# Kernel tuning notes

Measured on AMD Instinct MI355X. Metric: run time of the kernel, lower is better.

The kernel has to match this reference:

```python
import jax, jax.numpy as jnp
import numpy as np

N = 50000      # nodes
E = 800000     # edges (before self-loops)
IN = 64        # in_dim
C = 64         # hidden_dim (per-head out channels)
H = 4          # heads
NEG_SLOPE = 0.2


def setup_inputs() -> dict:
    key = jax.random.key(0)
    ks = jax.random.split(key, 9)
    x = jax.random.normal(ks[0], (N, IN), jnp.float32)
    edge_index = jax.random.randint(ks[1], (2, E), 0, N)
    edge_attr = jax.random.uniform(ks[2], (E, 1), jnp.float32)
    s_in = 1.0 / np.sqrt(IN)
    s_c = 1.0 / np.sqrt(C)
    W = jax.random.normal(ks[3], (IN, H * C), jnp.float32) * s_in
    att_src = jax.random.normal(ks[4], (H, C), jnp.float32) * s_c
    att_dst = jax.random.normal(ks[5], (H, C), jnp.float32) * s_c
    lin_edge_w = jax.random.normal(ks[6], (1, H * C), jnp.float32)
    att_edge = jax.random.normal(ks[7], (H, C), jnp.float32) * s_c
    bias = jnp.zeros((C,), jnp.float32)
    return dict(x=x, edge_index=edge_index, edge_attr=edge_attr, W=W,
                att_src=att_src, att_dst=att_dst, lin_edge_w=lin_edge_w,
                att_edge=att_edge, bias=bias)


def reference(x, edge_index, edge_attr, W, att_src, att_dst, lin_edge_w, att_edge, bias):
    n = x.shape[0]
    # add self-loops (PyG default add_self_loops=True, fill_value='mean')
    loop = jnp.arange(n)
    src = jnp.concatenate([edge_index[0], loop])          # [E+N]
    dst = jnp.concatenate([edge_index[1], loop])          # [E+N]
    ea = jnp.concatenate([edge_attr,
                          jnp.full((n, 1), edge_attr.mean(), edge_attr.dtype)], axis=0)
    # node transform: [N, H, C]
    h = (x @ W).reshape(n, H, C)
    a_src = jnp.einsum('nhc,hc->nh', h, att_src)          # [N, H]
    a_dst = jnp.einsum('nhc,hc->nh', h, att_dst)          # [N, H]
    eh = (ea @ lin_edge_w).reshape(-1, H, C)              # [E+N, H, C]
    a_edge = jnp.einsum('ehc,hc->eh', eh, att_edge)       # [E+N, H]
    # per-edge attention logit
    alpha = a_src[src] + a_dst[dst] + a_edge              # [E+N, H]
    alpha = jax.nn.leaky_relu(alpha, NEG_SLOPE)
    # segment softmax over edges grouped by destination node
    amax = jax.ops.segment_max(alpha, dst, num_segments=n)
    alpha = jnp.exp(alpha - amax[dst])
    asum = jax.ops.segment_sum(alpha, dst, num_segments=n)
    alpha = alpha / (asum[dst] + 1e-16)                   # [E+N, H]
    # weighted message + scatter-add aggregation
    msg = h[src] * alpha[..., None]                       # [E+N, H, C]
    out = jax.ops.segment_sum(msg, dst, num_segments=n)   # [N, H, C]
    out = out.mean(axis=1) + bias                         # concat=False -> head mean
    # ReLU + residual
    return jax.nn.relu(out) + x
```

## Files before the change

kernel.cpp:

```cpp
#include <hip/hip_runtime.h>
#include <hip/hip_fp16.h>
#include <math.h>

#define H 4
#define C 64
#define HC 256
#define NEG 0.2f
#define ROWU 64
#define MAXREC 63
#define XPAD 72
#define HPAD 264
#define BKT 128
#define BSH 7
#define TILE 2048
#define SEG 32
#define SEGSH 5

typedef __attribute__((ext_vector_type(8))) _Float16 half8;
typedef __attribute__((ext_vector_type(4))) float f32x4;
typedef float f32x2 __attribute__((vector_size(8)));

__global__ __launch_bounds__(256) void phase1_kernel(
    const float* __restrict__ x, const float* __restrict__ W,
    const float* __restrict__ att_src, const float* __restrict__ att_dst,
    const int* __restrict__ ei, const float* __restrict__ edge_attr,
    unsigned char* __restrict__ h, float* __restrict__ a_src, float* __restrict__ a_dst,
    uint2* __restrict__ arena, unsigned* __restrict__ counts,
    float* __restrict__ mean_acc, int Nn, int Ee, int G1, int ntile) {
    int t = threadIdx.x;
    if ((int)blockIdx.x < G1) {
        __shared__ __align__(16) _Float16 xs[16 * XPAD];
        __shared__ __align__(16) _Float16 hs[16 * HPAD];
        int w = t >> 6, lane = t & 63, quad = lane >> 4, c16 = lane & 15;
        half8 bf[4][2];
#pragma unroll
        for (int nt = 0; nt < 4; ++nt)
#pragma unroll
            for (int kh = 0; kh < 2; ++kh)
#pragma unroll
                for (int j = 0; j < 8; ++j)
                    bf[nt][kh][j] = (_Float16)W[(kh * 32 + quad * 8 + j) * HC +
                                                w * 64 + nt * 16 + c16];
        float ats[4], atd[4];
#pragma unroll
        for (int nt = 0; nt < 4; ++nt) {
            ats[nt] = att_src[w * 64 + nt * 16 + c16];
            atd[nt] = att_dst[w * 64 + nt * 16 + c16];
        }

        int nTiles = (Nn + 15) >> 4;
        for (int mt = blockIdx.x; mt < nTiles; mt += G1) {
            __syncthreads();
            {
                int row = t >> 4, col4 = (t & 15) * 4;
                int node = mt * 16 + row;
                float4 v = make_float4(0.f, 0.f, 0.f, 0.f);
                if (node < Nn) v = *(const float4*)(x + (size_t)node * 64 + col4);
                _Float16* dst = xs + row * XPAD + col4;
                dst[0] = (_Float16)v.x; dst[1] = (_Float16)v.y;
                dst[2] = (_Float16)v.z; dst[3] = (_Float16)v.w;
            }
            __syncthreads();
            half8 a0 = *(const half8*)(xs + c16 * XPAD + quad * 8);
            half8 a1 = *(const half8*)(xs + c16 * XPAD + 32 + quad * 8);
            f32x4 d[4];
#pragma unroll
            for (int nt = 0; nt < 4; ++nt) {
                f32x4 acc = {0.f, 0.f, 0.f, 0.f};
                acc = __builtin_amdgcn_mfma_f32_16x16x32_f16(a0, bf[nt][0], acc, 0, 0, 0);
                acc = __builtin_amdgcn_mfma_f32_16x16x32_f16(a1, bf[nt][1], acc, 0, 0, 0);
                d[nt] = acc;
            }
#pragma unroll
            for (int reg = 0; reg < 4; ++reg) {
                float ps = 0.f, pd = 0.f;
#pragma unroll
                for (int nt = 0; nt < 4; ++nt) {
                    ps += d[nt][reg] * ats[nt];
                    pd += d[nt][reg] * atd[nt];
                }
                ps += __shfl_xor(ps, 1); pd += __shfl_xor(pd, 1);
                ps += __shfl_xor(ps, 2); pd += __shfl_xor(pd, 2);
                ps += __shfl_xor(ps, 4); pd += __shfl_xor(pd, 4);
                ps += __shfl_xor(ps, 8); pd += __shfl_xor(pd, 8);
                if (c16 == 0) {
                    int node = mt * 16 + quad * 4 + reg;
                    if (node < Nn) {
                        a_src[node * 4 + w] = ps;
                        a_dst[node * 4 + w] = pd;
                    }
                }
            }
#pragma unroll
            for (int nt = 0; nt < 4; ++nt)
#pragma unroll
                for (int reg = 0; reg < 4; ++reg)
                    hs[(quad * 4 + reg) * HPAD + w * 64 + nt * 16 + c16] =
                        (_Float16)d[nt][reg];
            __syncthreads();
            {
                int row = t >> 4, chunk = t & 15;
                int node = mt * 16 + row;
                if (node < Nn) {
                    const uint4* sp = (const uint4*)(hs + row * HPAD + chunk * 16);
                    uint4 sA = sp[0], sB = sp[1];
                    unsigned ua[8] = {sA.x, sA.y, sA.z, sA.w, sB.x, sB.y, sB.z, sB.w};
                    unsigned ow[4];
#pragma unroll
                    for (int q = 0; q < 4; ++q) {
                        float2 p0 = __half22float2(*reinterpret_cast<const __half2*>(&ua[q * 2]));
                        float2 p1 = __half22float2(*reinterpret_cast<const __half2*>(&ua[q * 2 + 1]));
                        int v = __builtin_amdgcn_cvt_pk_fp8_f32(p0.x, p0.y, 0, false);
                        v = __builtin_amdgcn_cvt_pk_fp8_f32(p1.x, p1.y, v, true);
                        ow[q] = (unsigned)v;
                    }
                    *(uint4*)(h + (size_t)node * HC + chunk * 16) =
                        make_uint4(ow[0], ow[1], ow[2], ow[3]);
                }
            }
        }
    } else {
        __shared__ float red[256];
        __shared__ unsigned cntA[512];
        int nbkt = (Nn + BKT - 1) >> BSH;
        int tile = (int)blockIdx.x - G1;
        for (int bb = t; bb < nbkt; bb += 256) cntA[bb] = 0;
        __syncthreads();
        int e0 = tile * TILE;
        size_t tbase = (size_t)tile * nbkt;
        float s = 0.f;
#pragma unroll 4
        for (int k = 0; k < TILE / 256; ++k) {
            int i = e0 + k * 256 + t;
            if (i < Ee) {
                int src = ei[i];
                int dst = ei[Ee + i];
                float ea = edge_attr[i];
                s += ea;
                unsigned q = (unsigned)(ea * 65535.f + 0.5f);
                int b = dst >> BSH;
                unsigned r = atomicAdd(&cntA[b], 1u);
                if (r < SEG)
                    arena[(tbase + b) * SEG + r] =
                        make_uint2((q << 16) | (unsigned)src,
                                   (unsigned)(dst & (BKT - 1)));
            }
        }
        __syncthreads();
        for (int bb = t; bb < nbkt; bb += 256) {
            unsigned c = cntA[bb];
            counts[tbase + bb] = c < (unsigned)SEG ? c : (unsigned)SEG;
        }
        red[t] = s;
        __syncthreads();
        for (int o = 128; o; o >>= 1) {
            if (t < o) red[t] += red[t + o];
            __syncthreads();
        }
        if (t == 0) atomicAdd(mean_acc, red[0]);
    }
}

__global__ __launch_bounds__(256) void bucket_kernel(
    const uint2* __restrict__ arena, const unsigned* __restrict__ counts,
    unsigned* __restrict__ edges, int ntile, int nbkt) {
    __shared__ unsigned rows[BKT * ROWU];
    __shared__ unsigned cnt[BKT];
    __shared__ unsigned short segc[512];
    int b = blockIdx.x, t = threadIdx.x;
    if (t < BKT) cnt[t] = 0;
    for (int j = t; j < ntile; j += 256)
        segc[j] = (unsigned short)counts[(size_t)j * nbkt + b];
    __syncthreads();
    int total = ntile * SEG;
    for (int j = t; j < total; j += 256) {
        int seg = j >> SEGSH, slot = j & (SEG - 1);
        if (slot < (int)segc[seg]) {
            uint2 e = arena[((size_t)seg * nbkt + b) * SEG + slot];
            unsigned r = atomicAdd(&cnt[e.y], 1u);
            if (r < MAXREC) rows[e.y * ROWU + 1 + r] = e.x;
        }
    }
    __syncthreads();
    if (t < BKT) rows[t * ROWU] = cnt[t] < (unsigned)MAXREC ? cnt[t] : (unsigned)MAXREC;
    __syncthreads();
    size_t obase = (size_t)b * (BKT * ROWU);
    for (int i = t; i < BKT * (ROWU / 4); i += 256)
        *(uint4*)(edges + obase + i * 4) = *(const uint4*)(rows + i * 4);
}

__global__ __launch_bounds__(256) void aggregate_kernel(
    const unsigned* __restrict__ edges,
    const float* __restrict__ a_src, const float* __restrict__ a_dst,
    const float* __restrict__ lin_edge_w, const float* __restrict__ att_edge,
    const float* __restrict__ mean_acc, const unsigned char* __restrict__ h,
    const float* __restrict__ bias, const float* __restrict__ x,
    float* __restrict__ out, int Nn, float invE) {
    int lane = threadIdx.x & 63;
    int n = blockIdx.x * 4 + (threadIdx.x >> 6);
    if (n >= Nn) return;
    int head = lane >> 4;
    int sub = lane & 15;

    size_t rowbase = (size_t)n * ROWU;
    unsigned deg = edges[rowbase];
    unsigned rec = edges[rowbase + 1 + lane];
    const unsigned* h8 = (const unsigned*)h;
    unsigned sv = h8[(size_t)n * 64 + lane];
    float mean = mean_acc[0] * invE;
    float ad = a_dst[n * 4 + head];
    float asn = a_src[n * 4 + head];

    float kp = 0.f;
#pragma unroll
    for (int j = 0; j < 4; ++j) {
        int c = sub * 4 + j;
        kp += lin_edge_w[head * C + c] * att_edge[head * C + c];
    }
    kp += __shfl_xor(kp, 1);
    kp += __shfl_xor(kp, 2);
    kp += __shfl_xor(kp, 4);
    kp += __shfl_xor(kp, 8);
    float K = kp;
    const float DEQ = 1.0f / 65535.f;

    if (deg > MAXREC) deg = MAXREC;

    float wk0, wk1, wk2, wk3;
    {
        float wtmp[4];
#pragma unroll
        for (int k = 0; k < 4; ++k) {
            int e = sub + 16 * k;
            unsigned re = (unsigned)__shfl((int)rec, e);
            int se = (e < (int)deg) ? (int)(re & 0xFFFF) : 0;
            float lg = a_src[se * 4 + head] + ad + (float)(re >> 16) * DEQ * K;
            lg = lg > 0.f ? lg : NEG * lg;
            wtmp[k] = (e < (int)deg) ? __expf(lg) : 0.f;
        }
        wk0 = wtmp[0]; wk1 = wtmp[1]; wk2 = wtmp[2]; wk3 = wtmp[3];
    }
    float sw = (wk0 + wk1) + (wk2 + wk3);
    sw += __shfl_xor(sw, 1);
    sw += __shfl_xor(sw, 2);
    sw += __shfl_xor(sw, 4);
    sw += __shfl_xor(sw, 8);

    float ls = asn + ad + mean * K;
    ls = ls > 0.f ? ls : NEG * ls;
    float wsl = __expf(ls);
    f32x2 s01 = __builtin_amdgcn_cvt_pk_f32_fp8((int)sv, false);
    f32x2 s23 = __builtin_amdgcn_cvt_pk_f32_fp8((int)sv, true);
    float4 acc = make_float4(wsl * s01[0], wsl * s01[1], wsl * s23[0], wsl * s23[1]);
    float swgt = sw + wsl;
    int hb = lane & 48;

#pragma unroll
    for (int k = 0; k < 4; ++k) {
        int base = k * 16;
        if (base >= (int)deg) break;
        float wsrc = (k == 0) ? wk0 : (k == 1) ? wk1 : (k == 2) ? wk2 : wk3;
        int cnt = (int)deg - base;
        if (cnt > 16) cnt = 16;
        int j = 0;
        for (; j + 4 <= cnt; j += 4) {
            int e0 = base + j;
            unsigned r0 = (unsigned)__builtin_amdgcn_readlane((int)rec, e0 + 0);
            unsigned r1 = (unsigned)__builtin_amdgcn_readlane((int)rec, e0 + 1);
            unsigned r2 = (unsigned)__builtin_amdgcn_readlane((int)rec, e0 + 2);
            unsigned r3 = (unsigned)__builtin_amdgcn_readlane((int)rec, e0 + 3);
            unsigned hv0 = h8[(size_t)(r0 & 0xFFFF) * 64 + lane];
            unsigned hv1 = h8[(size_t)(r1 & 0xFFFF) * 64 + lane];
            unsigned hv2 = h8[(size_t)(r2 & 0xFFFF) * 64 + lane];
            unsigned hv3 = h8[(size_t)(r3 & 0xFFFF) * 64 + lane];
            float w0 = __shfl(wsrc, hb | (j + 0));
            float w1 = __shfl(wsrc, hb | (j + 1));
            float w2 = __shfl(wsrc, hb | (j + 2));
            float w3 = __shfl(wsrc, hb | (j + 3));
            {
                f32x2 f01 = __builtin_amdgcn_cvt_pk_f32_fp8((int)hv0, false);
                f32x2 f23 = __builtin_amdgcn_cvt_pk_f32_fp8((int)hv0, true);
                acc.x += w0 * f01[0]; acc.y += w0 * f01[1];
                acc.z += w0 * f23[0]; acc.w += w0 * f23[1];
            }
            {
                f32x2 f01 = __builtin_amdgcn_cvt_pk_f32_fp8((int)hv1, false);
                f32x2 f23 = __builtin_amdgcn_cvt_pk_f32_fp8((int)hv1, true);
                acc.x += w1 * f01[0]; acc.y += w1 * f01[1];
                acc.z += w1 * f23[0]; acc.w += w1 * f23[1];
            }
            {
                f32x2 f01 = __builtin_amdgcn_cvt_pk_f32_fp8((int)hv2, false);
                f32x2 f23 = __builtin_amdgcn_cvt_pk_f32_fp8((int)hv2, true);
                acc.x += w2 * f01[0]; acc.y += w2 * f01[1];
                acc.z += w2 * f23[0]; acc.w += w2 * f23[1];
            }
            {
                f32x2 f01 = __builtin_amdgcn_cvt_pk_f32_fp8((int)hv3, false);
                f32x2 f23 = __builtin_amdgcn_cvt_pk_f32_fp8((int)hv3, true);
                acc.x += w3 * f01[0]; acc.y += w3 * f01[1];
                acc.z += w3 * f23[0]; acc.w += w3 * f23[1];
            }
        }
        for (; j < cnt; ++j) {
            unsigned r = (unsigned)__builtin_amdgcn_readlane((int)rec, base + j);
            unsigned hv = h8[(size_t)(r & 0xFFFF) * 64 + lane];
            float wg = __shfl(wsrc, hb | j);
            f32x2 f01 = __builtin_amdgcn_cvt_pk_f32_fp8((int)hv, false);
            f32x2 f23 = __builtin_amdgcn_cvt_pk_f32_fp8((int)hv, true);
            acc.x += wg * f01[0]; acc.y += wg * f01[1];
            acc.z += wg * f23[0]; acc.w += wg * f23[1];
        }
    }

    float inv = 1.f / (swgt + 1e-16f);
    acc.x *= inv; acc.y *= inv; acc.z *= inv; acc.w *= inv;

    acc.x += __shfl_xor(acc.x, 16);
    acc.y += __shfl_xor(acc.y, 16);
    acc.z += __shfl_xor(acc.z, 16);
    acc.w += __shfl_xor(acc.w, 16);
    acc.x += __shfl_xor(acc.x, 32);
    acc.y += __shfl_xor(acc.y, 32);
    acc.z += __shfl_xor(acc.z, 32);
    acc.w += __shfl_xor(acc.w, 32);
    if (lane < 16) {
        float4 b = ((const float4*)bias)[lane];
        float4 xv = ((const float4*)x)[(size_t)n * 16 + lane];
        float4 o;
        o.x = fmaxf(acc.x * 0.25f + b.x, 0.f) + xv.x;
        o.y = fmaxf(acc.y * 0.25f + b.y, 0.f) + xv.y;
        o.z = fmaxf(acc.z * 0.25f + b.z, 0.f) + xv.z;
        o.w = fmaxf(acc.w * 0.25f + b.w, 0.f) + xv.w;
        ((float4*)out)[(size_t)n * 16 + lane] = o;
    }
}

extern "C" void kernel_launch(void* const* d_in, const int* in_sizes, int n_in,
                              void* d_out, int out_size, void* d_ws, size_t ws_size,
                              hipStream_t stream) {
    const float* x = (const float*)d_in[0];
    const int* ei = (const int*)d_in[1];
    const float* edge_attr = (const float*)d_in[2];
    const float* W = (const float*)d_in[3];
    const float* att_src = (const float*)d_in[4];
    const float* att_dst = (const float*)d_in[5];
    const float* lin_edge_w = (const float*)d_in[6];
    const float* att_edge = (const float*)d_in[7];
    const float* bias = (const float*)d_in[8];
    float* out = (float*)d_out;
    int Nn = in_sizes[0] / 64;
    int Ee = in_sizes[1] / 2;
    int NB = (Nn + BKT - 1) >> BSH;
    int ntile = (Ee + TILE - 1) / TILE;

    char* p = (char*)d_ws;
    size_t off = 0;
    auto alloc = [&](size_t bytes) -> char* {
        char* r = p + off;
        off += (bytes + 255) & ~(size_t)255;
        return r;
    };
    float* mean_acc = (float*)alloc(256);
    size_t zero_bytes = off;
    unsigned* counts = (unsigned*)alloc((size_t)ntile * NB * 4);
    uint2* arena = (uint2*)alloc((size_t)ntile * NB * SEG * 8);
    unsigned* edges = (unsigned*)alloc((size_t)NB * BKT * ROWU * 4);
    unsigned char* h = (unsigned char*)alloc((size_t)Nn * HC);
    float* a_src = (float*)alloc((size_t)Nn * H * 4);
    float* a_dst = (float*)alloc((size_t)Nn * H * 4);
    (void)ws_size;

    const int G1 = 512;
    hipMemsetAsync(d_ws, 0, zero_bytes, stream);
    phase1_kernel<<<G1 + ntile, 256, 0, stream>>>(x, W, att_src, att_dst, ei, edge_attr,
                                                  h, a_src, a_dst, arena, counts,
                                                  mean_acc, Nn, Ee, G1, ntile);
    bucket_kernel<<<NB, 256, 0, stream>>>(arena, counts, edges, ntile, NB);
    aggregate_kernel<<<(Nn + 3) / 4, 256, 0, stream>>>(edges, a_src, a_dst,
                                                       lin_edge_w, att_edge, mean_acc,
                                                       h, bias, x, out, Nn,
                                                       1.0f / (float)Ee);
}
```

Before: 161.9 us.

## Regroup kernels: scatter alone, co-schedule GEMM with bucketing; batch gathers by eight

The edge-scatter work moves into its own kernel. The node-transform GEMM blocks now share a launch with the bucket-compaction blocks, using one shared-memory union, so the GEMM overlaps with bucketing instead of with scatter. G1 rises from 512 to 768. The aggregate loop now issues eight independent gathers before consuming them, to increase memory-level parallelism. The cost is a larger shared allocation for the GEMM blocks, which may reduce occupancy, plus per-element weight selection inside the loop.

```diff
diff --git a/kernel.cpp b/kernel.cpp
--- a/kernel.cpp
+++ b/kernel.cpp
@@ -15,22 +15,68 @@
 #define TILE 2048
 #define SEG 32
 #define SEGSH 5
+#define G1 768
 
 typedef __attribute__((ext_vector_type(8))) _Float16 half8;
 typedef __attribute__((ext_vector_type(4))) float f32x4;
 typedef float f32x2 __attribute__((vector_size(8)));
 
-__global__ __launch_bounds__(256) void phase1_kernel(
+__global__ __launch_bounds__(256) void scatter_kernel(
+    const int* __restrict__ ei, const float* __restrict__ edge_attr,
+    uint2* __restrict__ arena, unsigned* __restrict__ counts,
+    float* __restrict__ mean_acc, int Nn, int Ee, int ntile) {
+    __shared__ float red[256];
+    __shared__ unsigned cntA[512];
+    int t = threadIdx.x;
+    int nbkt = (Nn + BKT - 1) >> BSH;
+    int tile = (int)blockIdx.x;
+    for (int bb = t; bb < nbkt; bb += 256) cntA[bb] = 0;
+    __syncthreads();
+    int e0 = tile * TILE;
+    size_t tbase = (size_t)tile * nbkt;
+    float s = 0.f;
+#pragma unroll 4
+    for (int k = 0; k < TILE / 256; ++k) {
+        int i = e0 + k * 256 + t;
+        if (i < Ee) {
+            int src = ei[i];
+            int dst = ei[Ee + i];
+            float ea = edge_attr[i];
+            s += ea;
+            unsigned q = (unsigned)(ea * 65535.f + 0.5f);
+            int b = dst >> BSH;
+            unsigned r = atomicAdd(&cntA[b], 1u);
+            if (r < SEG)
+                arena[(tbase + b) * SEG + r] =
+                    make_uint2((q << 16) | (unsigned)src,
+                               (unsigned)(dst & (BKT - 1)));
+        }
+    }
+    __syncthreads();
+    for (int bb = t; bb < nbkt; bb += 256) {
+        unsigned c = cntA[bb];
+        counts[tbase + bb] = c < (unsigned)SEG ? c : (unsigned)SEG;
+    }
+    red[t] = s;
+    __syncthreads();
+    for (int o = 128; o; o >>= 1) {
+        if (t < o) red[t] += red[t + o];
+        __syncthreads();
+    }
+    if (t == 0) atomicAdd(mean_acc, red[0]);
+}
+
+__global__ __launch_bounds__(256) void fused_kernel(
     const float* __restrict__ x, const float* __restrict__ W,
     const float* __restrict__ att_src, const float* __restrict__ att_dst,
-    const int* __restrict__ ei, const float* __restrict__ edge_attr,
     unsigned char* __restrict__ h, float* __restrict__ a_src, float* __restrict__ a_dst,
-    uint2* __restrict__ arena, unsigned* __restrict__ counts,
-    float* __restrict__ mean_acc, int Nn, int Ee, int G1, int ntile) {
+    const uint2* __restrict__ arena, const unsigned* __restrict__ counts,
+    unsigned* __restrict__ edges, int Nn, int ntile, int nbkt) {
+    __shared__ __align__(16) char smem[BKT * ROWU * 4 + BKT * 4 + 1024];
     int t = threadIdx.x;
     if ((int)blockIdx.x < G1) {
-        __shared__ __align__(16) _Float16 xs[16 * XPAD];
-        __shared__ __align__(16) _Float16 hs[16 * HPAD];
+        _Float16* xs = (_Float16*)smem;
+        _Float16* hs = (_Float16*)(smem + 16 * XPAD * 2);
         int w = t >> 6, lane = t & 63, quad = lane >> 4, c16 = lane & 15;
         half8 bf[4][2];
 #pragma unroll
@@ -120,73 +166,30 @@
             }
         }
     } else {
-        __shared__ float red[256];
-        __shared__ unsigned cntA[512];
-        int nbkt = (Nn + BKT - 1) >> BSH;
-        int tile = (int)blockIdx.x - G1;
-        for (int bb = t; bb < nbkt; bb += 256) cntA[bb] = 0;
+        unsigned* rows = (unsigned*)smem;
+        unsigned* cnt = (unsigned*)(smem + BKT * ROWU * 4);
+        unsigned short* segc = (unsigned short*)(smem + BKT * ROWU * 4 + BKT * 4);
+        int b = (int)blockIdx.x - G1;
+        if (t < BKT) cnt[t] = 0;
+        for (int j = t; j < ntile; j += 256)
+            segc[j] = (unsigned short)counts[(size_t)j * nbkt + b];
         __syncthreads();
-        int e0 = tile * TILE;
-        size_t tbase = (size_t)tile * nbkt;
-        float s = 0.f;
-#pragma unroll 4
-        for (int k = 0; k < TILE / 256; ++k) {
-            int i = e0 + k * 256 + t;
-            if (i < Ee) {
-                int src = ei[i];
-                int dst = ei[Ee + i];
-                float ea = edge_attr[i];
-                s += ea;
-                unsigned q = (unsigned)(ea * 65535.f + 0.5f);
-                int b = dst >> BSH;
-                unsigned r = atomicAdd(&cntA[b], 1u);
-                if (r < SEG)
-                    arena[(tbase + b) * SEG + r] =
-                        make_uint2((q << 16) | (unsigned)src,
-                                   (unsigned)(dst & (BKT - 1)));
+        int total = ntile * SEG;
+        for (int j = t; j < total; j += 256) {
+            int seg = j >> SEGSH, slot = j & (SEG - 1);
+            if (slot < (int)segc[seg]) {
+                uint2 e = arena[((size_t)seg * nbkt + b) * SEG + slot];
+                unsigned r = atomicAdd(&cnt[e.y], 1u);
+                if (r < MAXREC) rows[e.y * ROWU + 1 + r] = e.x;
             }
         }
         __syncthreads();
-        for (int bb = t; bb < nbkt; bb += 256) {
-            unsigned c = cntA[bb];
-            counts[tbase + bb] = c < (unsigned)SEG ? c : (unsigned)SEG;
-        }
-        red[t] = s;
+        if (t < BKT) rows[t * ROWU] = cnt[t] < (unsigned)MAXREC ? cnt[t] : (unsigned)MAXREC;
         __syncthreads();
-        for (int o = 128; o; o >>= 1) {
-            if (t < o) red[t] += red[t + o];
-            __syncthreads();
-        }
-        if (t == 0) atomicAdd(mean_acc, red[0]);
-    }
-}
-
-__global__ __launch_bounds__(256) void bucket_kernel(
-    const uint2* __restrict__ arena, const unsigned* __restrict__ counts,
-    unsigned* __restrict__ edges, int ntile, int nbkt) {
-    __shared__ unsigned rows[BKT * ROWU];
-    __shared__ unsigned cnt[BKT];
-    __shared__ unsigned short segc[512];
-    int b = blockIdx.x, t = threadIdx.x;
-    if (t < BKT) cnt[t] = 0;
-    for (int j = t; j < ntile; j += 256)
-        segc[j] = (unsigned short)counts[(size_t)j * nbkt + b];
-    __syncthreads();
-    int total = ntile * SEG;
-    for (int j = t; j < total; j += 256) {
-        int seg = j >> SEGSH, slot = j & (SEG - 1);
-        if (slot < (int)segc[seg]) {
-            uint2 e = arena[((size_t)seg * nbkt + b) * SEG + slot];
-            unsigned r = atomicAdd(&cnt[e.y], 1u);
-            if (r < MAXREC) rows[e.y * ROWU + 1 + r] = e.x;
-        }
-    }
-    __syncthreads();
-    if (t < BKT) rows[t * ROWU] = cnt[t] < (unsigned)MAXREC ? cnt[t] : (unsigned)MAXREC;
-    __syncthreads();
-    size_t obase = (size_t)b * (BKT * ROWU);
-    for (int i = t; i < BKT * (ROWU / 4); i += 256)
-        *(uint4*)(edges + obase + i * 4) = *(const uint4*)(rows + i * 4);
+        size_t obase = (size_t)b * (BKT * ROWU);
+        for (int i = t; i < BKT * (ROWU / 4); i += 256)
+            *(uint4*)(edges + obase + i * 4) = *(const uint4*)(rows + i * 4);
+    }
 }
 
 __global__ __launch_bounds__(256) void aggregate_kernel(
@@ -255,62 +258,32 @@
     float swgt = sw + wsl;
     int hb = lane & 48;
 
-#pragma unroll
-    for (int k = 0; k < 4; ++k) {
-        int base = k * 16;
-        if (base >= (int)deg) break;
-        float wsrc = (k == 0) ? wk0 : (k == 1) ? wk1 : (k == 2) ? wk2 : wk3;
-        int cnt = (int)deg - base;
-        if (cnt > 16) cnt = 16;
-        int j = 0;
-        for (; j + 4 <= cnt; j += 4) {
-            int e0 = base + j;
-            unsigned r0 = (unsigned)__builtin_amdgcn_readlane((int)rec, e0 + 0);
-            unsigned r1 = (unsigned)__builtin_amdgcn_readlane((int)rec, e0 + 1);
-            unsigned r2 = (unsigned)__builtin_amdgcn_readlane((int)rec, e0 + 2);
-            unsigned r3 = (unsigned)__builtin_amdgcn_readlane((int)rec, e0 + 3);
-            unsigned hv0 = h8[(size_t)(r0 & 0xFFFF) * 64 + lane];
-            unsigned hv1 = h8[(size_t)(r1 & 0xFFFF) * 64 + lane];
-            unsigned hv2 = h8[(size_t)(r2 & 0xFFFF) * 64 + lane];
-            unsigned hv3 = h8[(size_t)(r3 & 0xFFFF) * 64 + lane];
-            float w0 = __shfl(wsrc, hb | (j + 0));
-            float w1 = __shfl(wsrc, hb | (j + 1));
-            float w2 = __shfl(wsrc, hb | (j + 2));
-            float w3 = __shfl(wsrc, hb | (j + 3));
-            {
-                f32x2 f01 = __builtin_amdgcn_cvt_pk_f32_fp8((int)hv0, false);
-                f32x2 f23 = __builtin_amdgcn_cvt_pk_f32_fp8((int)hv0, true);
-                acc.x += w0 * f01[0]; acc.y += w0 * f01[1];
-                acc.z += w0 * f23[0]; acc.w += w0 * f23[1];
-            }
-            {
-                f32x2 f01 = __builtin_amdgcn_cvt_pk_f32_fp8((int)hv1, false);
-                f32x2 f23 = __builtin_amdgcn_cvt_pk_f32_fp8((int)hv1, true);
-                acc.x += w1 * f01[0]; acc.y += w1 * f01[1];
-                acc.z += w1 * f23[0]; acc.w += w1 * f23[1];
-            }
-            {
-                f32x2 f01 = __builtin_amdgcn_cvt_pk_f32_fp8((int)hv2, false);
-                f32x2 f23 = __builtin_amdgcn_cvt_pk_f32_fp8((int)hv2, true);
-                acc.x += w2 * f01[0]; acc.y += w2 * f01[1];
-                acc.z += w2 * f23[0]; acc.w += w2 * f23[1];
-            }
-            {
-                f32x2 f01 = __builtin_amdgcn_cvt_pk_f32_fp8((int)hv3, false);
-                f32x2 f23 = __builtin_amdgcn_cvt_pk_f32_fp8((int)hv3, true);
-                acc.x += w3 * f01[0]; acc.y += w3 * f01[1];
-                acc.z += w3 * f23[0]; acc.w += w3 * f23[1];
-            }
-        }
-        for (; j < cnt; ++j) {
-            unsigned r = (unsigned)__builtin_amdgcn_readlane((int)rec, base + j);
-            unsigned hv = h8[(size_t)(r & 0xFFFF) * 64 + lane];
-            float wg = __shfl(wsrc, hb | j);
-            f32x2 f01 = __builtin_amdgcn_cvt_pk_f32_fp8((int)hv, false);
-            f32x2 f23 = __builtin_amdgcn_cvt_pk_f32_fp8((int)hv, true);
-            acc.x += wg * f01[0]; acc.y += wg * f01[1];
-            acc.z += wg * f23[0]; acc.w += wg * f23[1];
-        }
+    for (int g = 0; g < (int)deg; g += 8) {
+        int cnt = (int)deg - g;
+        if (cnt > 8) cnt = 8;
+        unsigned hv0 = 0, hv1 = 0, hv2 = 0, hv3 = 0, hv4 = 0, hv5 = 0, hv6 = 0, hv7 = 0;
+#define GATH(u, dst)                                                          \
+        if (u < cnt) {                                                        \
+            unsigned r = (unsigned)__builtin_amdgcn_readlane((int)rec, g + u);\
+            dst = h8[(size_t)(r & 0xFFFF) * 64 + lane];                       \
+        }
+        GATH(0, hv0) GATH(1, hv1) GATH(2, hv2) GATH(3, hv3)
+        GATH(4, hv4) GATH(5, hv5) GATH(6, hv6) GATH(7, hv7)
+#undef GATH
+#define CONS(u, src)                                                          \
+        if (u < cnt) {                                                        \
+            int e = g + u;                                                    \
+            int k = e >> 4;                                                   \
+            float wsrc = (k == 0) ? wk0 : (k == 1) ? wk1 : (k == 2) ? wk2 : wk3; \
+            float wg = __shfl(wsrc, hb | (e & 15));                           \
+            f32x2 f01 = __builtin_amdgcn_cvt_pk_f32_fp8((int)src, false);     \
+            f32x2 f23 = __builtin_amdgcn_cvt_pk_f32_fp8((int)src, true);      \
+            acc.x += wg * f01[0]; acc.y += wg * f01[1];                       \
+            acc.z += wg * f23[0]; acc.w += wg * f23[1];                       \
+        }
+        CONS(0, hv0) CONS(1, hv1) CONS(2, hv2) CONS(3, hv3)
+        CONS(4, hv4) CONS(5, hv5) CONS(6, hv6) CONS(7, hv7)
+#undef CONS
     }
 
     float inv = 1.f / (swgt + 1e-16f);
@@ -371,12 +344,12 @@
     float* a_dst = (float*)alloc((size_t)Nn * H * 4);
     (void)ws_size;
 
-    const int G1 = 512;
     hipMemsetAsync(d_ws, 0, zero_bytes, stream);
-    phase1_kernel<<<G1 + ntile, 256, 0, stream>>>(x, W, att_src, att_dst, ei, edge_attr,
-                                                  h, a_src, a_dst, arena, counts,
-                                                  mean_acc, Nn, Ee, G1, ntile);
-    bucket_kernel<<<NB, 256, 0, stream>>>(arena, counts, edges, ntile, NB);
+    scatter_kernel<<<ntile, 256, 0, stream>>>(ei, edge_attr, arena, counts,
+                                              mean_acc, Nn, Ee, ntile);
+    fused_kernel<<<G1 + NB, 256, 0, stream>>>(x, W, att_src, att_dst,
+                                              h, a_src, a_dst, arena, counts,
+                                              edges, Nn, ntile, NB);
     aggregate_kernel<<<(Nn + 3) / 4, 256, 0, stream>>>(edges, a_src, a_dst,
                                                        lin_edge_w, att_edge, mean_acc,
                                                        h, bias, x, out, Nn,
```

Measured after the change: 167.7 us. +3.6%, slower.
